# Performance work log

Hardware: AMD Instinct MI355X
Metric: run time of the kernel (lower is better)

Reference implementation:

```python
import jax, jax.numpy as jnp
from jax import lax
import numpy as np

N, L, E, NHEAD, DFF = 16, 1024, 512, 8, 2048
HD = E // NHEAD
NLEVELS = 10  # log2(1024)
S_SCALES = NLEVELS + 1


def setup_inputs() -> dict:
    key = jax.random.key(0)
    ks = jax.random.split(key, 12)
    s = 0.05
    return {
        "src": jax.random.normal(ks[0], (N, L, E), jnp.float32),
        "conv_w": jax.random.normal(ks[1], (NLEVELS, HD, HD, 2), jnp.float32) * s,
        "conv_b": jax.random.normal(ks[2], (NLEVELS, HD), jnp.float32) * s,
        "in_proj_w": jax.random.normal(ks[3], (3 * E, E), jnp.float32) * s,
        "in_proj_b": jax.random.normal(ks[4], (3 * E,), jnp.float32) * s,
        "out_proj_w": jax.random.normal(ks[5], (E, E), jnp.float32) * s,
        "out_proj_b": jax.random.normal(ks[6], (E,), jnp.float32) * s,
        "ln1_w": jnp.ones((E,), jnp.float32),
        "ln1_b": jnp.zeros((E,), jnp.float32),
        "ln2_w": jnp.ones((E,), jnp.float32),
        "ln2_b": jnp.zeros((E,), jnp.float32),
        "w1": jax.random.normal(ks[7], (DFF, E), jnp.float32) * s,
        "b1": jax.random.normal(ks[8], (DFF,), jnp.float32) * s,
        "w2": jax.random.normal(ks[9], (E, DFF), jnp.float32) * s,
        "b2": jax.random.normal(ks[10], (E,), jnp.float32) * s,
    }


def _layer_norm(x, w, b, eps=1e-5):
    mu = jnp.mean(x, axis=-1, keepdims=True)
    var = jnp.mean(jnp.square(x - mu), axis=-1, keepdims=True)
    return (x - mu) * lax.rsqrt(var + eps) * w + b


def _forward(src, conv_w, conv_b, in_proj_w, in_proj_b, out_proj_w, out_proj_b,
             ln1_w, ln1_b, ln2_w, ln2_b, w1, b1, w2, b2):
    n, l, e = src.shape
    hd = e // NHEAD
    # pyramid over 1D spatial dim, channels-first
    out = jnp.transpose(src, (0, 2, 1))  # (N, E, L)
    hidden_vals = [out]
    for i in range(NLEVELS):
        x = out.reshape(n * NHEAD, hd, out.shape[-1])  # (N*H, hd, li)
        x = lax.conv_general_dilated(
            x, conv_w[i], window_strides=(2,), padding='VALID',
            dimension_numbers=('NCH', 'OIH', 'NCH'))
        x = jax.nn.relu(x + conv_b[i][None, :, None])
        out = x.reshape(n, e, x.shape[-1])  # (N, E, li/2)
        # upsample back to full length via repeat_interleave
        hidden_vals.append(jnp.repeat(out, l // out.shape[-1], axis=2))
    hv = jnp.stack(hidden_vals, -1)                      # (N, E, L, S)
    s = hv.shape[-1]
    hv = jnp.transpose(hv, (3, 0, 2, 1)).reshape(s, n * l, e)  # (S, N*L, E)

    # multi-head attention: length-1 query (finest scale) over all scales
    b_ = n * l
    q = hv[0:1] @ in_proj_w[:e].T + in_proj_b[:e]            # (1, B, E)
    k = hv @ in_proj_w[e:2 * e].T + in_proj_b[e:2 * e]       # (S, B, E)
    v = hv @ in_proj_w[2 * e:].T + in_proj_b[2 * e:]         # (S, B, E)
    qh = jnp.transpose(q.reshape(1, b_, NHEAD, hd), (1, 2, 0, 3))  # (B, H, 1, hd)
    kh = jnp.transpose(k.reshape(s, b_, NHEAD, hd), (1, 2, 0, 3))  # (B, H, S, hd)
    vh = jnp.transpose(v.reshape(s, b_, NHEAD, hd), (1, 2, 0, 3))  # (B, H, S, hd)
    scores = jnp.einsum('bhqd,bhkd->bhqk', qh, kh) / jnp.sqrt(jnp.float32(hd))
    attn = jax.nn.softmax(scores, axis=-1)
    o = jnp.einsum('bhqk,bhkd->bhqd', attn, vh)              # (B, H, 1, hd)
    o = o.reshape(b_, e) @ out_proj_w.T + out_proj_b         # (B, E)
    src2 = o.reshape(n, l, e)

    # faithful to source: residual computed then overwritten by norm1(src2)
    x = _layer_norm(src2, ln1_w, ln1_b)
    ff = jax.nn.relu(x @ w1.T + b1) @ w2.T + b2
    return _layer_norm(x + ff, ln2_w, ln2_b)


def reference(src, conv_w, conv_b, in_proj_w, in_proj_b, out_proj_w, out_proj_b,
              ln1_w, ln1_b, ln2_w, ln2_b, w1, b1, w2, b2):
    return _forward(src, conv_w, conv_b, in_proj_w, in_proj_b, out_proj_w,
                    out_proj_b, ln1_w, ln1_b, ln2_w, ln2_b, w1, b1, w2, b2)
```

## Files before the change

### kernel.cpp

```cpp
#include <hip/hip_runtime.h>
#include <hip/hip_bf16.h>
#include <stdint.h>
#include <math.h>

#define NB      16
#define LL      1024
#define EE      512
#define NHEADS  8
#define DFF     2048
#define NLEVELS 10
#define NSCALES 11
#define BROWS   (NB * LL)

typedef unsigned short u16;
typedef __attribute__((ext_vector_type(8))) short bf16x8;
typedef __attribute__((ext_vector_type(4))) float f32x4;

static const size_t B_SRCBF = 0;
static const size_t B_LVLBF = 16777216;
static const size_t B_QKV   = 33538048;
static const size_t B_KVS   = 83869696;
static const size_t B_OBF   = 117391360;
static const size_t B_X     = 134168576;
static const size_t B_XBF   = 167723008;
static const size_t B_WBF   = 184500224;
static const size_t B_FFH   = 0;

__device__ __forceinline__ u16 f2bf(float x) {
    union { float f; uint32_t u; } c; c.f = x;
    uint32_t u = c.u + 0x7FFFu + ((c.u >> 16) & 1u);
    return (u16)(u >> 16);
}
__device__ __forceinline__ float bf2f(u16 v) {
    union { uint32_t u; float f; } c; c.u = ((uint32_t)v) << 16; return c.f;
}
__device__ __forceinline__ void ld8bf(const u16* p, float* f) {
    uint4 r = *(const uint4*)p;
    uint32_t ws[4] = { r.x, r.y, r.z, r.w };
    #pragma unroll
    for (int j = 0; j < 4; j++) {
        union { uint32_t u; float g; } lo, hi;
        lo.u = ws[j] << 16; hi.u = ws[j] & 0xFFFF0000u;
        f[2 * j] = lo.g; f[2 * j + 1] = hi.g;
    }
}
__device__ __forceinline__ void gload16(const u16* g, u16* l) {
    __builtin_amdgcn_global_load_lds(
        (const __attribute__((address_space(1))) void*)g,
        (__attribute__((address_space(3))) void*)l, 16, 0, 0);
}

__global__ void cast_all_kernel(const float* __restrict__ s0, const float* __restrict__ s1,
                                const float* __restrict__ s2, const float* __restrict__ s3,
                                const float* __restrict__ s4, const float* __restrict__ cw,
                                u16* __restrict__ d0, u16* __restrict__ d1,
                                u16* __restrict__ d2, u16* __restrict__ d3,
                                u16* __restrict__ d4, u16* __restrict__ dw)
{
    int bid = blockIdx.x;
    if (bid >= 11264) {
        int base = (bid - 11264) * 1024 + threadIdx.x * 4;
        #pragma unroll
        for (int j = 0; j < 4; j++) {
            int idx = base + j;
            int lvl = idx >> 13, rem = idx & 8191;
            int o = rem >> 7, ck = rem & 127;
            int k = ck >> 6, ci = ck & 63;
            dw[idx] = f2bf(cw[(lvl << 13) + (o << 7) + (ci << 1) + k]);
        }
        return;
    }
    const float* s; u16* d; int nt;
    if      (bid < 8192)  { s = s0; d = d0; nt = 2097152; }
    else if (bid < 8960)  { bid -= 8192;  s = s1; d = d1; nt = 196608; }
    else if (bid < 9216)  { bid -= 8960;  s = s2; d = d2; nt = 65536;  }
    else if (bid < 10240) { bid -= 9216;  s = s3; d = d3; nt = 262144; }
    else                  { bid -= 10240; s = s4; d = d4; nt = 262144; }
    int i = bid * 256 + threadIdx.x;
    if (i < nt) {
        float4 v = ((const float4*)s)[i];
        uint2 o;
        o.x = (uint32_t)f2bf(v.x) | ((uint32_t)f2bf(v.y) << 16);
        o.y = (uint32_t)f2bf(v.z) | ((uint32_t)f2bf(v.w) << 16);
        ((uint2*)d)[i] = o;
    }
}

__global__ __launch_bounds__(256, 2)
void conv_chain_kernel(const u16* __restrict__ src_bf, u16* __restrict__ lvl_bf,
                       const u16* __restrict__ cw, const float* __restrict__ cb)
{
    __shared__ u16 BIG[16384];
    __shared__ u16 MID[8192];
    __shared__ u16 WB[8192];
    const int tid = threadIdx.x;
    const int l = tid & 63, w = tid >> 6;
    const int bid = blockIdx.x;
    const int q  = bid & 3;
    const int h  = (bid >> 2) & 7;
    const int n  = bid >> 5;

    {
        const u16* base = src_bf + ((size_t)n * 1024 + q * 256) * 512 + h * 64;
        #pragma unroll
        for (int j = 0; j < 8; j++) {
            int c = j * 256 + w * 64 + l;
            int row = c >> 3, lch = c & 7;
            int gch = lch ^ (row & 7);
            gload16(base + (size_t)row * 512 + gch * 8,
                    BIG + (size_t)(j * 256 + w * 64) * 8);
        }
    }

    const u16* IN = BIG;
    u16* OUTb = MID;
    int R = 128;
    int T = 512;
    size_t rowOff = 0;
    for (int lvl = 1; lvl <= 8; lvl++) {
        {
            const u16* wsrc = cw + (size_t)(lvl - 1) * 8192;
            #pragma unroll
            for (int j = 0; j < 4; j++) {
                int c = j * 256 + w * 64 + l;
                int o = c >> 4, lch = c & 15;
                int gch = lch ^ (o & 7);
                gload16(wsrc + o * 128 + gch * 8, WB + (size_t)(j * 256 + w * 64) * 8);
            }
        }
        asm volatile("s_waitcnt vmcnt(0)" ::: "memory");
        __syncthreads();

        const int nrt = (R + 15) >> 4;
        const int maxil = 2 * R - 1;
        for (int f = w; f < nrt * 4; f += 4) {
            int rt = f >> 2, nc = f & 3;
            int o = nc * 16 + (l & 15);
            f32x4 acc = {0.f, 0.f, 0.f, 0.f};
            #pragma unroll
            for (int s = 0; s < 4; s++) {
                int il = 2 * (rt * 16 + (l & 15)) + (s >> 1);
                if (il > maxil) il = maxil;
                int ach = (((s & 1) * 4) + (l >> 4)) ^ (il & 7);
                bf16x8 av = *(const bf16x8*)(IN + il * 64 + ach * 8);
                int bch = (s * 4 + (l >> 4)) ^ (o & 7);
                bf16x8 bv = *(const bf16x8*)(WB + o * 128 + bch * 8);
                acc = __builtin_amdgcn_mfma_f32_16x16x32_bf16(av, bv, acc, 0, 0, 0);
            }
            float bb = cb[(lvl - 1) * 64 + o];
            #pragma unroll
            for (int reg = 0; reg < 4; reg++) {
                int rloc = rt * 16 + (l >> 4) * 4 + reg;
                if (rloc < R) {
                    float v = fmaxf(acc[reg] + bb, 0.f);
                    u16 b16 = f2bf(v);
                    lvl_bf[(rowOff + (size_t)n * T + (size_t)q * R + rloc) * 512 + h * 64 + o] = b16;
                    OUTb[rloc * 64 + (((o >> 3) ^ (rloc & 7)) << 3) + (o & 7)] = b16;
                }
            }
        }
        __syncthreads();
        const u16* tmp = IN; IN = OUTb; OUTb = (u16*)tmp;
        rowOff += (size_t)16 * T;
        T >>= 1; R >>= 1;
    }
}

__global__ void conv_tail_kernel(u16* __restrict__ lvl_bf, const u16* __restrict__ cw,
                                 const float* __restrict__ cb)
{
    const int h = blockIdx.x & 7, n = blockIdx.x >> 3;
    const int tid = threadIdx.x;
    __shared__ float L8s[4][64];
    __shared__ float L9s[2][64];
    {
        int r = tid >> 6, c = tid & 63;
        L8s[r][c] = bf2f(lvl_bf[((size_t)16256 + n * 4 + r) * 512 + h * 64 + c]);
    }
    __syncthreads();
    if (tid < 128) {
        int t = tid >> 6, o = tid & 63;
        const u16* wr = cw + (size_t)8 * 8192 + o * 128;
        float acc = cb[8 * 64 + o];
        #pragma unroll
        for (int k = 0; k < 2; k++)
            #pragma unroll 16
            for (int ci = 0; ci < 64; ci++)
                acc += L8s[2 * t + k][ci] * bf2f(wr[k * 64 + ci]);
        acc = fmaxf(acc, 0.f);
        L9s[t][o] = acc;
        lvl_bf[((size_t)16320 + n * 2 + t) * 512 + h * 64 + o] = f2bf(acc);
    }
    __syncthreads();
    if (tid < 64) {
        int o = tid;
        const u16* wr = cw + (size_t)9 * 8192 + o * 128;
        float acc = cb[9 * 64 + o];
        #pragma unroll
        for (int k = 0; k < 2; k++)
            #pragma unroll 16
            for (int ci = 0; ci < 64; ci++)
                acc += L9s[k][ci] * bf2f(wr[k * 64 + ci]);
        acc = fmaxf(acc, 0.f);
        lvl_bf[((size_t)16352 + n) * 512 + h * 64 + o] = f2bf(acc);
    }
}

__global__ __launch_bounds__(256, 3)
void mfma_gemm(const u16* __restrict__ A, const u16* __restrict__ W,
               const float* __restrict__ bias, const float* __restrict__ residual,
               const u16* __restrict__ resb,
               float* __restrict__ Cf, u16* __restrict__ Cb,
               int M, int K, int N, int relu, int gx)
{
    __shared__ u16 lds[24576];
    const int tid = threadIdx.x;
    const int l = tid & 63, w = tid >> 6;
    const int wm = w >> 1, wn = w & 1;

    const int nwg = gridDim.x;
    const int q = nwg >> 3, r = nwg & 7;
    const int xcd = blockIdx.x & 7, idx = blockIdx.x >> 3;
    const int lin = (xcd < r ? xcd * (q + 1) : r * (q + 1) + (xcd - r) * q) + idx;
    const int by = lin / gx, bx = lin - by * gx;
    const int rowBase = by * 128, colBase = bx * 128;

    f32x4 acc[4][4];
    #pragma unroll
    for (int m = 0; m < 4; m++)
        #pragma unroll
        for (int n = 0; n < 4; n++) acc[m][n] = 0.f;

    int rA0 = rowBase + w * 16 + (l >> 2);        if (rA0 > M - 1) rA0 = M - 1;
    int rA1 = rowBase + 64 + w * 16 + (l >> 2);   if (rA1 > M - 1) rA1 = M - 1;
    const u16* gA0 = A + (size_t)rA0 * K + (l & 3) * 8;
    const u16* gA1 = A + (size_t)rA1 * K + (l & 3) * 8;
    const u16* gB0 = W + (size_t)(colBase + w * 16 + (l >> 2)) * K + (l & 3) * 8;
    const u16* gB1 = W + (size_t)(colBase + 64 + w * 16 + (l >> 2)) * K + (l & 3) * 8;

    const int NT = K >> 5;
    auto STAGE = [&](int tt, int buf) {
        const int kb = tt << 5;
        u16* d = lds + buf * 8192 + w * 512;
        gload16(gA0 + kb, d);
        gload16(gA1 + kb, d + 2048);
        gload16(gB0 + kb, d + 4096);
        gload16(gB1 + kb, d + 4096 + 2048);
    };
    STAGE(0, 0);
    if (NT > 1) STAGE(1, 1);

    int cbuf = 0;
    int sbuf = 2;
    for (int t = 0; t < NT; ++t) {
        if (t + 2 < NT) STAGE(t + 2, sbuf);
        const int rem = NT - 1 - t;
        if (rem >= 2)      asm volatile("s_waitcnt vmcnt(8)" ::: "memory");
        else if (rem == 1) asm volatile("s_waitcnt vmcnt(4)" ::: "memory");
        else               asm volatile("s_waitcnt vmcnt(0)" ::: "memory");
        __builtin_amdgcn_s_barrier();
        __builtin_amdgcn_sched_barrier(0);

        const u16* bufc = lds + cbuf * 8192;
        const u16* pa = bufc + (wm * 64 + (l & 15)) * 32 + (l >> 4) * 8;
        const u16* pb = bufc + 4096 + (wn * 64 + (l & 15)) * 32 + (l >> 4) * 8;
        bf16x8 av[4], bv[4];
        #pragma unroll
        for (int m = 0; m < 4; m++) av[m] = *(const bf16x8*)(pa + m * 512);
        #pragma unroll
        for (int n = 0; n < 4; n++) bv[n] = *(const bf16x8*)(pb + n * 512);
        #pragma unroll
        for (int m = 0; m < 4; m++)
            #pragma unroll
            for (int n = 0; n < 4; n++)
                acc[m][n] = __builtin_amdgcn_mfma_f32_16x16x32_bf16(av[m], bv[n], acc[m][n], 0, 0, 0);

        __builtin_amdgcn_sched_barrier(0);
        __builtin_amdgcn_s_barrier();
        __builtin_amdgcn_sched_barrier(0);

        cbuf = (cbuf == 2) ? 0 : cbuf + 1;
        sbuf = (sbuf == 2) ? 0 : sbuf + 1;
    }

    const int cc = colBase + wn * 64 + (l & 15);
    float bs4[4];
    #pragma unroll
    for (int n = 0; n < 4; n++) bs4[n] = bias[cc + n * 16];

    if (Cb) {
        u16* WS = lds + w * 2048;
        #pragma unroll
        for (int hh = 0; hh < 2; hh++) {
            #pragma unroll
            for (int mi = 0; mi < 2; mi++) {
                #pragma unroll
                for (int n = 0; n < 4; n++) {
                    int colv = n * 16 + (l & 15);
                    #pragma unroll
                    for (int reg = 0; reg < 4; reg++) {
                        int rowh = mi * 16 + (l >> 4) * 4 + reg;
                        float v = acc[hh * 2 + mi][n][reg] + bs4[n];
                        if (relu) v = fmaxf(v, 0.f);
                        WS[rowh * 64 + (colv ^ (((rowh >> 2) & 3) << 4))] = f2bf(v);
                    }
                }
            }
            asm volatile("s_waitcnt lgkmcnt(0)" ::: "memory");
            __builtin_amdgcn_sched_barrier(0);
            #pragma unroll
            for (int j = 0; j < 4; j++) {
                int rowh = (l >> 3) + 8 * j;
                int col8 = (l & 7) * 8;
                int colx = col8 ^ (((rowh >> 2) & 3) << 4);
                uint4 v = *(const uint4*)(WS + rowh * 64 + colx);
                int grow = rowBase + wm * 64 + hh * 32 + rowh;
                if (grow < M)
                    *(uint4*)(Cb + (size_t)grow * N + colBase + wn * 64 + col8) = v;
            }
        }
    } else {
        float* WSf = (float*)lds + w * 2048;
        #pragma unroll
        for (int hh = 0; hh < 2; hh++) {
            #pragma unroll
            for (int mi = 0; mi < 2; mi++) {
                #pragma unroll
                for (int n = 0; n < 4; n++) {
                    int colv = n * 16 + (l & 15);
                    #pragma unroll
                    for (int reg = 0; reg < 4; reg++) {
                        int rowh = mi * 16 + (l >> 4) * 4 + reg;
                        WSf[rowh * 64 + (colv ^ (((rowh >> 2) & 3) << 4))] =
                            acc[hh * 2 + mi][n][reg] + bs4[n];
                    }
                }
            }
            asm volatile("s_waitcnt lgkmcnt(0)" ::: "memory");
            __builtin_amdgcn_sched_barrier(0);
            #pragma unroll
            for (int j = 0; j < 8; j++) {
                int rowh = (l >> 4) + 4 * j;
                int col4 = (l & 15) * 4;
                int colx = col4 ^ (((rowh >> 2) & 3) << 4);
                float4 v = *(const float4*)(WSf + rowh * 64 + colx);
                int grow = rowBase + wm * 64 + hh * 32 + rowh;
                if (grow < M) {
                    int gcol = colBase + wn * 64 + col4;
                    if (residual) {
                        float4 rr = *(const float4*)&residual[(size_t)grow * N + gcol];
                        v.x += rr.x; v.y += rr.y; v.z += rr.z; v.w += rr.w;
                    }
                    if (resb) {
                        uint2 rb = *(const uint2*)&resb[(size_t)grow * N + gcol];
                        v.x += bf2f((u16)(rb.x & 0xFFFF));
                        v.y += bf2f((u16)(rb.x >> 16));
                        v.z += bf2f((u16)(rb.y & 0xFFFF));
                        v.w += bf2f((u16)(rb.y >> 16));
                    }
                    if (relu) {
                        v.x = fmaxf(v.x, 0.f); v.y = fmaxf(v.y, 0.f);
                        v.z = fmaxf(v.z, 0.f); v.w = fmaxf(v.w, 0.f);
                    }
                    *(float4*)&Cf[(size_t)grow * N + gcol] = v;
                }
            }
        }
    }
}

__global__ void attn_kernel(const u16* __restrict__ QKV, const u16* __restrict__ KVs,
                            u16* __restrict__ O)
{
    const int wv   = threadIdx.x >> 6;
    const int lane = threadIdx.x & 63;
    const int b    = blockIdx.x * 4 + wv;
    const int h    = lane >> 3;
    const int d8   = lane & 7;
    const int n = b >> 10, pos = b & 1023;

    float q[8];
    ld8bf(QKV + (size_t)b * 1536 + h * 64 + d8 * 8, q);

    float sc[NSCALES];
    {
        float kk[8];
        ld8bf(QKV + (size_t)b * 1536 + 512 + h * 64 + d8 * 8, kk);
        float p = 0.f;
        #pragma unroll
        for (int j = 0; j < 8; j++) p += q[j] * kk[j];
        p += __shfl_xor(p, 1); p += __shfl_xor(p, 2); p += __shfl_xor(p, 4);
        sc[0] = p * 0.125f;
    }
    {
        int rowOff = 0;
        #pragma unroll
        for (int s = 1; s <= NLEVELS; s++) {
            int Ls = 1024 >> s;
            int row = rowOff + n * Ls + (pos >> s);
            float kk[8];
            ld8bf(KVs + (size_t)row * 1024 + h * 64 + d8 * 8, kk);
            float p = 0.f;
            #pragma unroll
            for (int j = 0; j < 8; j++) p += q[j] * kk[j];
            p += __shfl_xor(p, 1); p += __shfl_xor(p, 2); p += __shfl_xor(p, 4);
            sc[s] = p * 0.125f;
            rowOff += 16 * Ls;
        }
    }
    float m = sc[0];
    #pragma unroll
    for (int s = 1; s < NSCALES; s++) m = fmaxf(m, sc[s]);
    float sum = 0.f;
    #pragma unroll
    for (int s = 0; s < NSCALES; s++) { sc[s] = __expf(sc[s] - m); sum += sc[s]; }
    float inv = 1.f / sum;

    float o[8] = {};
    {
        float vv[8];
        ld8bf(QKV + (size_t)b * 1536 + 1024 + h * 64 + d8 * 8, vv);
        float a = sc[0] * inv;
        #pragma unroll
        for (int j = 0; j < 8; j++) o[j] += a * vv[j];
    }
    {
        int rowOff = 0;
        #pragma unroll
        for (int s = 1; s <= NLEVELS; s++) {
            int Ls = 1024 >> s;
            int row = rowOff + n * Ls + (pos >> s);
            float vv[8];
            ld8bf(KVs + (size_t)row * 1024 + 512 + h * 64 + d8 * 8, vv);
            float a = sc[s] * inv;
            #pragma unroll
            for (int j = 0; j < 8; j++) o[j] += a * vv[j];
            rowOff += 16 * Ls;
        }
    }
    uint4 pk;
    pk.x = (uint32_t)f2bf(o[0]) | ((uint32_t)f2bf(o[1]) << 16);
    pk.y = (uint32_t)f2bf(o[2]) | ((uint32_t)f2bf(o[3]) << 16);
    pk.z = (uint32_t)f2bf(o[4]) | ((uint32_t)f2bf(o[5]) << 16);
    pk.w = (uint32_t)f2bf(o[6]) | ((uint32_t)f2bf(o[7]) << 16);
    *(uint4*)(O + (size_t)b * 512 + h * 64 + d8 * 8) = pk;
}

__global__ void ln_kernel(const float* __restrict__ in, float* __restrict__ out,
                          const float* __restrict__ w, const float* __restrict__ b,
                          u16* __restrict__ out_bf)
{
    const int l = threadIdx.x & 63;
    const int row = blockIdx.x * 4 + (threadIdx.x >> 6);
    const float* p = in + (size_t)row * EE + l * 8;
    float4 v0 = *(const float4*)p;
    float4 v1 = *(const float4*)(p + 4);
    float s  = v0.x + v0.y + v0.z + v0.w + v1.x + v1.y + v1.z + v1.w;
    float s2 = v0.x * v0.x + v0.y * v0.y + v0.z * v0.z + v0.w * v0.w
             + v1.x * v1.x + v1.y * v1.y + v1.z * v1.z + v1.w * v1.w;
    #pragma unroll
    for (int m = 1; m < 64; m <<= 1) { s += __shfl_xor(s, m); s2 += __shfl_xor(s2, m); }
    float mu  = s * (1.f / 512.f);
    float var = s2 * (1.f / 512.f) - mu * mu;
    float rs  = rsqrtf(var + 1e-5f);
    float4 w0 = *(const float4*)&w[l * 8], w1 = *(const float4*)&w[l * 8 + 4];
    float4 b0 = *(const float4*)&b[l * 8], b1 = *(const float4*)&b[l * 8 + 4];
    float o[8];
    o[0] = (v0.x - mu) * rs * w0.x + b0.x;
    o[1] = (v0.y - mu) * rs * w0.y + b0.y;
    o[2] = (v0.z - mu) * rs * w0.z + b0.z;
    o[3] = (v0.w - mu) * rs * w0.w + b0.w;
    o[4] = (v1.x - mu) * rs * w1.x + b1.x;
    o[5] = (v1.y - mu) * rs * w1.y + b1.y;
    o[6] = (v1.z - mu) * rs * w1.z + b1.z;
    o[7] = (v1.w - mu) * rs * w1.w + b1.w;
    float* po = out + (size_t)row * EE + l * 8;
    *(float4*)po       = make_float4(o[0], o[1], o[2], o[3]);
    *(float4*)(po + 4) = make_float4(o[4], o[5], o[6], o[7]);
    if (out_bf) {
        uint4 pk;
        pk.x = (uint32_t)f2bf(o[0]) | ((uint32_t)f2bf(o[1]) << 16);
        pk.y = (uint32_t)f2bf(o[2]) | ((uint32_t)f2bf(o[3]) << 16);
        pk.z = (uint32_t)f2bf(o[4]) | ((uint32_t)f2bf(o[5]) << 16);
        pk.w = (uint32_t)f2bf(o[6]) | ((uint32_t)f2bf(o[7]) << 16);
        *(uint4*)(out_bf + (size_t)row * EE + l * 8) = pk;
    }
}

extern "C" void kernel_launch(void* const* d_in, const int* in_sizes, int n_in,
                              void* d_out, int out_size, void* d_ws, size_t ws_size,
                              hipStream_t stream)
{
    const float* src        = (const float*)d_in[0];
    const float* conv_w     = (const float*)d_in[1];
    const float* conv_b     = (const float*)d_in[2];
    const float* in_proj_w  = (const float*)d_in[3];
    const float* in_proj_b  = (const float*)d_in[4];
    const float* out_proj_w = (const float*)d_in[5];
    const float* out_proj_b = (const float*)d_in[6];
    const float* ln1_w      = (const float*)d_in[7];
    const float* ln1_b      = (const float*)d_in[8];
    const float* ln2_w      = (const float*)d_in[9];
    const float* ln2_b      = (const float*)d_in[10];
    const float* w1         = (const float*)d_in[11];
    const float* b1         = (const float*)d_in[12];
    const float* w2         = (const float*)d_in[13];
    const float* b2         = (const float*)d_in[14];

    char*  wsb    = (char*)d_ws;
    float* out    = (float*)d_out;
    u16*   src_bf = (u16*)(wsb + B_SRCBF);
    u16*   lvl_bf = (u16*)(wsb + B_LVLBF);
    u16*   QKV    = (u16*)(wsb + B_QKV);
    u16*   KVs    = (u16*)(wsb + B_KVS);
    u16*   O_bf   = (u16*)(wsb + B_OBF);
    float* X      = (float*)(wsb + B_X);
    u16*   X_bf   = (u16*)(wsb + B_XBF);
    u16*   inw_bf = (u16*)(wsb + B_WBF);
    u16*   outw_bf= inw_bf + 786432;
    u16*   w1_bf  = outw_bf + 262144;
    u16*   w2_bf  = w1_bf + 1048576;
    u16*   cw_bf  = w2_bf + 1048576;
    u16*   FFH    = (u16*)(wsb + B_FFH);

    cast_all_kernel<<<11344, 256, 0, stream>>>(src, in_proj_w, out_proj_w, w1, w2, conv_w,
                                               src_bf, inw_bf, outw_bf, w1_bf, w2_bf, cw_bf);

    conv_chain_kernel<<<NB * NHEADS * 4, 256, 0, stream>>>(src_bf, lvl_bf, cw_bf, conv_b);
    conv_tail_kernel<<<NB * NHEADS, 256, 0, stream>>>(lvl_bf, cw_bf, conv_b);

    mfma_gemm<<<12 * 128, 256, 0, stream>>>(
        src_bf, inw_bf, in_proj_b, nullptr, nullptr, nullptr, QKV, BROWS, EE, 1536, 0, 12);

    mfma_gemm<<<8 * 128, 256, 0, stream>>>(
        lvl_bf, inw_bf + (size_t)512 * 512, in_proj_b + 512, nullptr, nullptr, nullptr, KVs,
        16368, EE, 1024, 0, 8);

    attn_kernel<<<BROWS / 4, 256, 0, stream>>>(QKV, KVs, O_bf);

    mfma_gemm<<<4 * 128, 256, 0, stream>>>(
        O_bf, outw_bf, out_proj_b, nullptr, nullptr, X, nullptr, BROWS, EE, EE, 0, 4);

    ln_kernel<<<BROWS / 4, 256, 0, stream>>>(X, X, ln1_w, ln1_b, X_bf);

    mfma_gemm<<<16 * 128, 256, 0, stream>>>(
        X_bf, w1_bf, b1, nullptr, nullptr, nullptr, FFH, BROWS, EE, DFF, 1, 16);

    mfma_gemm<<<4 * 128, 256, 0, stream>>>(
        FFH, w2_bf, b2, nullptr, X_bf, out, nullptr, BROWS, DFF, EE, 0, 4);

    ln_kernel<<<BROWS / 4, 256, 0, stream>>>(out, out, ln2_w, ln2_b, nullptr);
}
```

Measured before the change: 264.9 us.

## Enlarge GEMM tile to 256x128 with 8 waves, BK=64 and swizzled LDS

Restructures the bf16 MFMA GEMM from 128x128 tiles with 4 waves and K-step 32 to 256x128 tiles with 8 waves and K-step 64. It also switches from triple to double buffering and adds an XOR swizzle on the LDS chunk layout. The aim is more data reuse per loaded byte, fewer loop iterations and barriers, and fewer LDS bank conflicts. In exchange, LDS use per block rises to 96KB, which likely limits each CU to one resident block, and prefetch depth is halved.

```diff
diff --git a/kernel.cpp b/kernel.cpp
--- a/kernel.cpp
+++ b/kernel.cpp
@@ -206,14 +206,14 @@
     }
 }
 
-__global__ __launch_bounds__(256, 3)
+__global__ __launch_bounds__(512, 2)
 void mfma_gemm(const u16* __restrict__ A, const u16* __restrict__ W,
                const float* __restrict__ bias, const float* __restrict__ residual,
                const u16* __restrict__ resb,
                float* __restrict__ Cf, u16* __restrict__ Cb,
                int M, int K, int N, int relu, int gx)
 {
-    __shared__ u16 lds[24576];
+    __shared__ u16 lds[49152];
     const int tid = threadIdx.x;
     const int l = tid & 63, w = tid >> 6;
     const int wm = w >> 1, wn = w & 1;
@@ -223,7 +223,7 @@
     const int xcd = blockIdx.x & 7, idx = blockIdx.x >> 3;
     const int lin = (xcd < r ? xcd * (q + 1) : r * (q + 1) + (xcd - r) * q) + idx;
     const int by = lin / gx, bx = lin - by * gx;
-    const int rowBase = by * 128, colBase = bx * 128;
+    const int rowBase = by * 256, colBase = bx * 128;
 
     f32x4 acc[4][4];
     #pragma unroll
@@ -231,56 +231,75 @@
         #pragma unroll
         for (int n = 0; n < 4; n++) acc[m][n] = 0.f;
 
-    int rA0 = rowBase + w * 16 + (l >> 2);        if (rA0 > M - 1) rA0 = M - 1;
-    int rA1 = rowBase + 64 + w * 16 + (l >> 2);   if (rA1 > M - 1) rA1 = M - 1;
-    const u16* gA0 = A + (size_t)rA0 * K + (l & 3) * 8;
-    const u16* gA1 = A + (size_t)rA1 * K + (l & 3) * 8;
-    const u16* gB0 = W + (size_t)(colBase + w * 16 + (l >> 2)) * K + (l & 3) * 8;
-    const u16* gB1 = W + (size_t)(colBase + 64 + w * 16 + (l >> 2)) * K + (l & 3) * 8;
-
-    const int NT = K >> 5;
-    auto STAGE = [&](int tt, int buf) {
-        const int kb = tt << 5;
-        u16* d = lds + buf * 8192 + w * 512;
-        gload16(gA0 + kb, d);
-        gload16(gA1 + kb, d + 2048);
-        gload16(gB0 + kb, d + 4096);
-        gload16(gB1 + kb, d + 4096 + 2048);
+    const u16* gApt[4];
+    const u16* gBpt[2];
+    #pragma unroll
+    for (int i = 0; i < 4; i++) {
+        int c = (i * 8 + w) * 64 + l;
+        int row = c >> 3, lch = c & 7;
+        int gch = lch ^ ((row & 1) << 2);
+        int grow = rowBase + row; if (grow > M - 1) grow = M - 1;
+        gApt[i] = A + (size_t)grow * K + gch * 8;
+    }
+    #pragma unroll
+    for (int i = 0; i < 2; i++) {
+        int c = (i * 8 + w) * 64 + l;
+        int row = c >> 3, lch = c & 7;
+        int gch = lch ^ ((row & 1) << 2);
+        gBpt[i] = W + (size_t)(colBase + row) * K + gch * 8;
+    }
+
+    const int NT = K >> 6;
+    auto STAGE = [&](int tt) {
+        const int kb = tt << 6;
+        u16* dA = lds + (tt & 1) * 24576;
+        u16* dB = dA + 16384;
+        #pragma unroll
+        for (int i = 0; i < 4; i++)
+            gload16(gApt[i] + kb, dA + (size_t)(i * 8 + w) * 512);
+        #pragma unroll
+        for (int i = 0; i < 2; i++)
+            gload16(gBpt[i] + kb, dB + (size_t)(i * 8 + w) * 512);
     };
-    STAGE(0, 0);
-    if (NT > 1) STAGE(1, 1);
-
-    int cbuf = 0;
-    int sbuf = 2;
+    STAGE(0);
+
     for (int t = 0; t < NT; ++t) {
-        if (t + 2 < NT) STAGE(t + 2, sbuf);
-        const int rem = NT - 1 - t;
-        if (rem >= 2)      asm volatile("s_waitcnt vmcnt(8)" ::: "memory");
-        else if (rem == 1) asm volatile("s_waitcnt vmcnt(4)" ::: "memory");
-        else               asm volatile("s_waitcnt vmcnt(0)" ::: "memory");
+        if (t + 1 < NT) {
+            STAGE(t + 1);
+            asm volatile("s_waitcnt vmcnt(6)" ::: "memory");
+        } else {
+            asm volatile("s_waitcnt vmcnt(0)" ::: "memory");
+        }
         __builtin_amdgcn_s_barrier();
         __builtin_amdgcn_sched_barrier(0);
 
-        const u16* bufc = lds + cbuf * 8192;
-        const u16* pa = bufc + (wm * 64 + (l & 15)) * 32 + (l >> 4) * 8;
-        const u16* pb = bufc + 4096 + (wn * 64 + (l & 15)) * 32 + (l >> 4) * 8;
-        bf16x8 av[4], bv[4];
-        #pragma unroll
-        for (int m = 0; m < 4; m++) av[m] = *(const bf16x8*)(pa + m * 512);
-        #pragma unroll
-        for (int n = 0; n < 4; n++) bv[n] = *(const bf16x8*)(pb + n * 512);
-        #pragma unroll
-        for (int m = 0; m < 4; m++)
-            #pragma unroll
-            for (int n = 0; n < 4; n++)
-                acc[m][n] = __builtin_amdgcn_mfma_f32_16x16x32_bf16(av[m], bv[n], acc[m][n], 0, 0, 0);
+        const u16* Ab = lds + (t & 1) * 24576;
+        const u16* Bb = Ab + 16384;
+        #pragma unroll
+        for (int ks = 0; ks < 2; ks++) {
+            bf16x8 av[4], bv[4];
+            #pragma unroll
+            for (int fr = 0; fr < 4; fr++) {
+                int row = wm * 64 + fr * 16 + (l & 15);
+                int j = ks * 4 + (l >> 4);
+                av[fr] = *(const bf16x8*)(Ab + row * 64 + ((j ^ ((row & 1) << 2)) * 8));
+            }
+            #pragma unroll
+            for (int fc = 0; fc < 4; fc++) {
+                int col = wn * 64 + fc * 16 + (l & 15);
+                int j = ks * 4 + (l >> 4);
+                bv[fc] = *(const bf16x8*)(Bb + col * 64 + ((j ^ ((col & 1) << 2)) * 8));
+            }
+            #pragma unroll
+            for (int m = 0; m < 4; m++)
+                #pragma unroll
+                for (int n = 0; n < 4; n++)
+                    acc[m][n] = __builtin_amdgcn_mfma_f32_16x16x32_bf16(av[m], bv[n], acc[m][n], 0, 0, 0);
+        }
 
         __builtin_amdgcn_sched_barrier(0);
         __builtin_amdgcn_s_barrier();
         __builtin_amdgcn_sched_barrier(0);
-
-        cbuf = (cbuf == 2) ? 0 : cbuf + 1;
-        sbuf = (sbuf == 2) ? 0 : sbuf + 1;
     }
 
     const int cc = colBase + wn * 64 + (l & 15);
@@ -529,24 +548,24 @@
     conv_chain_kernel<<<NB * NHEADS * 4, 256, 0, stream>>>(src_bf, lvl_bf, cw_bf, conv_b);
     conv_tail_kernel<<<NB * NHEADS, 256, 0, stream>>>(lvl_bf, cw_bf, conv_b);
 
-    mfma_gemm<<<12 * 128, 256, 0, stream>>>(
+    mfma_gemm<<<64 * 12, 512, 0, stream>>>(
         src_bf, inw_bf, in_proj_b, nullptr, nullptr, nullptr, QKV, BROWS, EE, 1536, 0, 12);
 
-    mfma_gemm<<<8 * 128, 256, 0, stream>>>(
+    mfma_gemm<<<64 * 8, 512, 0, stream>>>(
         lvl_bf, inw_bf + (size_t)512 * 512, in_proj_b + 512, nullptr, nullptr, nullptr, KVs,
         16368, EE, 1024, 0, 8);
 
     attn_kernel<<<BROWS / 4, 256, 0, stream>>>(QKV, KVs, O_bf);
 
-    mfma_gemm<<<4 * 128, 256, 0, stream>>>(
+    mfma_gemm<<<64 * 4, 512, 0, stream>>>(
         O_bf, outw_bf, out_proj_b, nullptr, nullptr, X, nullptr, BROWS, EE, EE, 0, 4);
 
     ln_kernel<<<BROWS / 4, 256, 0, stream>>>(X, X, ln1_w, ln1_b, X_bf);
 
-    mfma_gemm<<<16 * 128, 256, 0, stream>>>(
+    mfma_gemm<<<64 * 16, 512, 0, stream>>>(
         X_bf, w1_bf, b1, nullptr, nullptr, nullptr, FFH, BROWS, EE, DFF, 1, 16);
 
-    mfma_gemm<<<4 * 128, 256, 0, stream>>>(
+    mfma_gemm<<<64 * 4, 512, 0, stream>>>(
         FFH, w2_bf, b2, nullptr, X_bf, out, nullptr, BROWS, DFF, EE, 0, 4);
 
     ln_kernel<<<BROWS / 4, 256, 0, stream>>>(out, out, ln2_w, ln2_b, nullptr);
```

After: 300.8 us. 1.14x slower.

## Use 256x128 GEMM tiles with 8 waves and XOR-swizzled LDS layout

Applied to the files above, without the earlier changes.

The shared bf16 MFMA GEMM now uses 512-thread blocks covering 256x128 output tiles instead of 256 threads on 128x128. Each B tile is reused across twice as many rows, and the global-to-LDS staging is rewritten so each thread loads a contiguous 16-byte chunk with an XOR swizzle to reduce LDS bank conflicts. The fp32 epilogue now stages results in smaller per-wave chunks, and the unused fp32 residual argument is removed. The risks are higher LDS use per block (about 72KB for three buffers) and register pressure, which may lower occupancy.

```diff
diff --git a/kernel.cpp b/kernel.cpp
--- a/kernel.cpp
+++ b/kernel.cpp
@@ -206,14 +206,14 @@
     }
 }
 
-__global__ __launch_bounds__(256, 3)
+__global__ __launch_bounds__(512, 4)
 void mfma_gemm(const u16* __restrict__ A, const u16* __restrict__ W,
-               const float* __restrict__ bias, const float* __restrict__ residual,
+               const float* __restrict__ bias,
                const u16* __restrict__ resb,
                float* __restrict__ Cf, u16* __restrict__ Cb,
                int M, int K, int N, int relu, int gx)
 {
-    __shared__ u16 lds[24576];
+    __shared__ u16 lds[36864];
     const int tid = threadIdx.x;
     const int l = tid & 63, w = tid >> 6;
     const int wm = w >> 1, wn = w & 1;
@@ -223,7 +223,7 @@
     const int xcd = blockIdx.x & 7, idx = blockIdx.x >> 3;
     const int lin = (xcd < r ? xcd * (q + 1) : r * (q + 1) + (xcd - r) * q) + idx;
     const int by = lin / gx, bx = lin - by * gx;
-    const int rowBase = by * 128, colBase = bx * 128;
+    const int rowBase = by * 256, colBase = bx * 128;
 
     f32x4 acc[4][4];
     #pragma unroll
@@ -231,44 +231,59 @@
         #pragma unroll
         for (int n = 0; n < 4; n++) acc[m][n] = 0.f;
 
-    int rA0 = rowBase + w * 16 + (l >> 2);        if (rA0 > M - 1) rA0 = M - 1;
-    int rA1 = rowBase + 64 + w * 16 + (l >> 2);   if (rA1 > M - 1) rA1 = M - 1;
-    const u16* gA0 = A + (size_t)rA0 * K + (l & 3) * 8;
-    const u16* gA1 = A + (size_t)rA1 * K + (l & 3) * 8;
-    const u16* gB0 = W + (size_t)(colBase + w * 16 + (l >> 2)) * K + (l & 3) * 8;
-    const u16* gB1 = W + (size_t)(colBase + 64 + w * 16 + (l >> 2)) * K + (l & 3) * 8;
+    const u16* gApt[2];
+    const u16* gBpt;
+    #pragma unroll
+    for (int i = 0; i < 2; i++) {
+        int G = i * 512 + tid;
+        int row = G >> 2, p = G & 3;
+        int c = p ^ (row & 3);
+        int grow = rowBase + row; if (grow > M - 1) grow = M - 1;
+        gApt[i] = A + (size_t)grow * K + c * 8;
+    }
+    {
+        int G = tid;
+        int row = G >> 2, p = G & 3;
+        int c = p ^ (row & 3);
+        gBpt = W + (size_t)(colBase + row) * K + c * 8;
+    }
 
     const int NT = K >> 5;
     auto STAGE = [&](int tt, int buf) {
         const int kb = tt << 5;
-        u16* d = lds + buf * 8192 + w * 512;
-        gload16(gA0 + kb, d);
-        gload16(gA1 + kb, d + 2048);
-        gload16(gB0 + kb, d + 4096);
-        gload16(gB1 + kb, d + 4096 + 2048);
+        u16* dA = lds + buf * 12288;
+        u16* dB = dA + 8192;
+        gload16(gApt[0] + kb, dA + (size_t)(w * 64) * 8);
+        gload16(gApt[1] + kb, dA + (size_t)(512 + w * 64) * 8);
+        gload16(gBpt + kb, dB + (size_t)(w * 64) * 8);
     };
     STAGE(0, 0);
     if (NT > 1) STAGE(1, 1);
 
-    int cbuf = 0;
-    int sbuf = 2;
+    int cbuf = 0, sbuf = 2;
     for (int t = 0; t < NT; ++t) {
         if (t + 2 < NT) STAGE(t + 2, sbuf);
         const int rem = NT - 1 - t;
-        if (rem >= 2)      asm volatile("s_waitcnt vmcnt(8)" ::: "memory");
-        else if (rem == 1) asm volatile("s_waitcnt vmcnt(4)" ::: "memory");
+        if (rem >= 2)      asm volatile("s_waitcnt vmcnt(6)" ::: "memory");
+        else if (rem == 1) asm volatile("s_waitcnt vmcnt(3)" ::: "memory");
         else               asm volatile("s_waitcnt vmcnt(0)" ::: "memory");
         __builtin_amdgcn_s_barrier();
         __builtin_amdgcn_sched_barrier(0);
 
-        const u16* bufc = lds + cbuf * 8192;
-        const u16* pa = bufc + (wm * 64 + (l & 15)) * 32 + (l >> 4) * 8;
-        const u16* pb = bufc + 4096 + (wn * 64 + (l & 15)) * 32 + (l >> 4) * 8;
+        const u16* Ab = lds + cbuf * 12288;
+        const u16* Bb = Ab + 8192;
+        const int c = l >> 4;
         bf16x8 av[4], bv[4];
         #pragma unroll
-        for (int m = 0; m < 4; m++) av[m] = *(const bf16x8*)(pa + m * 512);
-        #pragma unroll
-        for (int n = 0; n < 4; n++) bv[n] = *(const bf16x8*)(pb + n * 512);
+        for (int fr = 0; fr < 4; fr++) {
+            int row = wm * 64 + fr * 16 + (l & 15);
+            av[fr] = *(const bf16x8*)(Ab + row * 32 + ((c ^ (row & 3)) * 8));
+        }
+        #pragma unroll
+        for (int fc = 0; fc < 4; fc++) {
+            int col = wn * 64 + fc * 16 + (l & 15);
+            bv[fc] = *(const bf16x8*)(Bb + col * 32 + ((c ^ (col & 3)) * 8));
+        }
         #pragma unroll
         for (int m = 0; m < 4; m++)
             #pragma unroll
@@ -318,9 +333,10 @@
                 if (grow < M)
                     *(uint4*)(Cb + (size_t)grow * N + colBase + wn * 64 + col8) = v;
             }
+            asm volatile("s_waitcnt lgkmcnt(0)" ::: "memory");
         }
     } else {
-        float* WSf = (float*)lds + w * 2048;
+        float* WSf = (float*)lds + w * 1024;
         #pragma unroll
         for (int hh = 0; hh < 2; hh++) {
             #pragma unroll
@@ -330,40 +346,37 @@
                     int colv = n * 16 + (l & 15);
                     #pragma unroll
                     for (int reg = 0; reg < 4; reg++) {
-                        int rowh = mi * 16 + (l >> 4) * 4 + reg;
+                        int rowh = (l >> 4) * 4 + reg;
                         WSf[rowh * 64 + (colv ^ (((rowh >> 2) & 3) << 4))] =
                             acc[hh * 2 + mi][n][reg] + bs4[n];
                     }
                 }
-            }
-            asm volatile("s_waitcnt lgkmcnt(0)" ::: "memory");
-            __builtin_amdgcn_sched_barrier(0);
-            #pragma unroll
-            for (int j = 0; j < 8; j++) {
-                int rowh = (l >> 4) + 4 * j;
-                int col4 = (l & 15) * 4;
-                int colx = col4 ^ (((rowh >> 2) & 3) << 4);
-                float4 v = *(const float4*)(WSf + rowh * 64 + colx);
-                int grow = rowBase + wm * 64 + hh * 32 + rowh;
-                if (grow < M) {
-                    int gcol = colBase + wn * 64 + col4;
-                    if (residual) {
-                        float4 rr = *(const float4*)&residual[(size_t)grow * N + gcol];
-                        v.x += rr.x; v.y += rr.y; v.z += rr.z; v.w += rr.w;
+                asm volatile("s_waitcnt lgkmcnt(0)" ::: "memory");
+                __builtin_amdgcn_sched_barrier(0);
+                #pragma unroll
+                for (int j = 0; j < 4; j++) {
+                    int rowh = (l >> 4) + 4 * j;
+                    int col4 = (l & 15) * 4;
+                    int colx = col4 ^ (((rowh >> 2) & 3) << 4);
+                    float4 v = *(const float4*)(WSf + rowh * 64 + colx);
+                    int grow = rowBase + wm * 64 + hh * 32 + mi * 16 + rowh;
+                    if (grow < M) {
+                        int gcol = colBase + wn * 64 + col4;
+                        if (resb) {
+                            uint2 rb = *(const uint2*)&resb[(size_t)grow * N + gcol];
+                            v.x += bf2f((u16)(rb.x & 0xFFFF));
+                            v.y += bf2f((u16)(rb.x >> 16));
+                            v.z += bf2f((u16)(rb.y & 0xFFFF));
+                            v.w += bf2f((u16)(rb.y >> 16));
+                        }
+                        if (relu) {
+                            v.x = fmaxf(v.x, 0.f); v.y = fmaxf(v.y, 0.f);
+                            v.z = fmaxf(v.z, 0.f); v.w = fmaxf(v.w, 0.f);
+                        }
+                        *(float4*)&Cf[(size_t)grow * N + gcol] = v;
                     }
-                    if (resb) {
-                        uint2 rb = *(const uint2*)&resb[(size_t)grow * N + gcol];
-                        v.x += bf2f((u16)(rb.x & 0xFFFF));
-                        v.y += bf2f((u16)(rb.x >> 16));
-                        v.z += bf2f((u16)(rb.y & 0xFFFF));
-                        v.w += bf2f((u16)(rb.y >> 16));
-                    }
-                    if (relu) {
-                        v.x = fmaxf(v.x, 0.f); v.y = fmaxf(v.y, 0.f);
-                        v.z = fmaxf(v.z, 0.f); v.w = fmaxf(v.w, 0.f);
-                    }
-                    *(float4*)&Cf[(size_t)grow * N + gcol] = v;
                 }
+                asm volatile("s_waitcnt lgkmcnt(0)" ::: "memory");
             }
         }
     }
@@ -529,25 +542,25 @@
     conv_chain_kernel<<<NB * NHEADS * 4, 256, 0, stream>>>(src_bf, lvl_bf, cw_bf, conv_b);
     conv_tail_kernel<<<NB * NHEADS, 256, 0, stream>>>(lvl_bf, cw_bf, conv_b);
 
-    mfma_gemm<<<12 * 128, 256, 0, stream>>>(
-        src_bf, inw_bf, in_proj_b, nullptr, nullptr, nullptr, QKV, BROWS, EE, 1536, 0, 12);
-
-    mfma_gemm<<<8 * 128, 256, 0, stream>>>(
-        lvl_bf, inw_bf + (size_t)512 * 512, in_proj_b + 512, nullptr, nullptr, nullptr, KVs,
+    mfma_gemm<<<64 * 12, 512, 0, stream>>>(
+        src_bf, inw_bf, in_proj_b, nullptr, nullptr, QKV, BROWS, EE, 1536, 0, 12);
+
+    mfma_gemm<<<64 * 8, 512, 0, stream>>>(
+        lvl_bf, inw_bf + (size_t)512 * 512, in_proj_b + 512, nullptr, nullptr, KVs,
         16368, EE, 1024, 0, 8);
 
     attn_kernel<<<BROWS / 4, 256, 0, stream>>>(QKV, KVs, O_bf);
 
-    mfma_gemm<<<4 * 128, 256, 0, stream>>>(
-        O_bf, outw_bf, out_proj_b, nullptr, nullptr, X, nullptr, BROWS, EE, EE, 0, 4);
+    mfma_gemm<<<64 * 4, 512, 0, stream>>>(
+        O_bf, outw_bf, out_proj_b, nullptr, X, nullptr, BROWS, EE, EE, 0, 4);
 
     ln_kernel<<<BROWS / 4, 256, 0, stream>>>(X, X, ln1_w, ln1_b, X_bf);
 
-    mfma_gemm<<<16 * 128, 256, 0, stream>>>(
-        X_bf, w1_bf, b1, nullptr, nullptr, nullptr, FFH, BROWS, EE, DFF, 1, 16);
-
-    mfma_gemm<<<4 * 128, 256, 0, stream>>>(
-        FFH, w2_bf, b2, nullptr, X_bf, out, nullptr, BROWS, DFF, EE, 0, 4);
+    mfma_gemm<<<64 * 16, 512, 0, stream>>>(
+        X_bf, w1_bf, b1, nullptr, nullptr, FFH, BROWS, EE, DFF, 1, 16);
+
+    mfma_gemm<<<64 * 4, 512, 0, stream>>>(
+        FFH, w2_bf, b2, X_bf, out, nullptr, BROWS, DFF, EE, 0, 4);
 
     ln_kernel<<<BROWS / 4, 256, 0, stream>>>(out, out, ln2_w, ln2_b, nullptr);
 }
```

New measurement: 262.8 us. Within noise of the previous version (-0.8%).
